# Kernel optimization log

Measured on AMD Instinct MI355X. Metric: run time of the kernel, lower is better.

The kernel has to match this reference:

```python
import jax, jax.numpy as jnp
import numpy as np

NEG_SLOPE = 0.2


def _gcn_conv(x, edge_index, W, b):
    # Standard GCNConv: y = D^-1/2 (A + I) D^-1/2 (x W) + b
    N = x.shape[0]
    loop = jnp.arange(N, dtype=edge_index.dtype)
    src = jnp.concatenate([edge_index[0], loop])  # [E+N]
    dst = jnp.concatenate([edge_index[1], loop])  # [E+N]
    deg = jax.ops.segment_sum(jnp.ones_like(dst, dtype=x.dtype), dst, num_segments=N)
    dinv = jnp.where(deg > 0, jax.lax.rsqrt(deg), 0.0)
    norm = dinv[src] * dinv[dst]                  # [E+N]
    h = x @ W                                     # [N, out] dense GEMM
    msg = h[src] * norm[:, None]                  # irregular gather, [E+N, out]
    agg = jax.ops.segment_sum(msg, dst, num_segments=N)  # irregular scatter
    return agg + b


def setup_inputs() -> dict:
    key = jax.random.key(0)
    ks = jax.random.split(key, 5)
    N, E, d_in, d_hid = 50000, 800000, 256, 512
    s = lambda fan_in, fan_out: np.sqrt(6.0 / (fan_in + fan_out))
    return {
        "x": jax.random.normal(ks[0], (N, d_in), dtype=jnp.float32),
        "edge_index": jax.random.randint(ks[1], (2, E), 0, N, dtype=jnp.int64),
        "W_gcn": jax.random.uniform(ks[2], (d_in, d_hid), jnp.float32, -s(d_in, d_hid), s(d_in, d_hid)),
        "b_gcn": jnp.zeros((d_hid,), jnp.float32),
        "W2": jax.random.uniform(ks[3], (d_hid, d_hid), jnp.float32, -s(d_hid, d_hid), s(d_hid, d_hid)),
        "b2": jnp.zeros((d_hid,), jnp.float32),
        "W_out": jax.random.uniform(ks[4], (d_hid, 1), jnp.float32, -s(d_hid, 1), s(d_hid, 1)),
        "b_out": jnp.zeros((1,), jnp.float32),
    }


def reference(x, edge_index, W_gcn, b_gcn, W2, b2, W_out, b_out):
    h = _gcn_conv(x, edge_index, W_gcn, b_gcn)           # [N, 512]
    h = jax.nn.leaky_relu(h, NEG_SLOPE)
    h = jax.nn.leaky_relu(h @ W2 + b2, NEG_SLOPE)        # [N, 512]
    return h @ W_out + b_out                             # [N, 1]
```

## Files before the change

kernel.cpp:

```cpp
#include <hip/hip_runtime.h>

#define D_IN  256
#define D_HID 512
#define NEG_SLOPE 0.2f
#define SCAN_CHUNK 2048

typedef __attribute__((ext_vector_type(8))) short short8;
typedef __attribute__((ext_vector_type(4))) float floatx4;

__device__ __forceinline__ unsigned short f2bf(float f) {
    unsigned int u = __float_as_uint(f);
    u += 0x7fffu + ((u >> 16) & 1u);
    return (unsigned short)(u >> 16);
}
__device__ __forceinline__ float bf2f(unsigned short u) {
    return __uint_as_float(((unsigned int)u) << 16);
}

__device__ __forceinline__ int eidx(const void* ei, long pos, int is64) {
    return is64 ? (int)((const long long*)ei)[pos] : ((const int*)ei)[pos];
}

__global__ __launch_bounds__(256) void k_init(const float* __restrict__ x,
                                              unsigned short* __restrict__ xb,
                                              int* __restrict__ deg, int N,
                                              const unsigned int* __restrict__ ei,
                                              int npairs, int* flag,
                                              const float* __restrict__ W_gcn,
                                              unsigned short* __restrict__ Wgt,
                                              const float* __restrict__ W2,
                                              unsigned short* __restrict__ W2t,
                                              const float* __restrict__ b_out,
                                              float* __restrict__ outacc,
                                              long xthreads) {
    long t = (long)blockIdx.x * blockDim.x + threadIdx.x;
    if (t < xthreads) {
        long i = t * 4;
        float4 v = *(const float4*)(x + i);
        ushort4 o;
        o.x = f2bf(v.x); o.y = f2bf(v.y); o.z = f2bf(v.z); o.w = f2bf(v.w);
        *(ushort4*)(xb + i) = o;
        if (t < N) deg[t] = 0;
        if (blockIdx.x == 0) {
            __shared__ int nz;
            if (threadIdx.x == 0) nz = 0;
            __syncthreads();
            for (int p = threadIdx.x; p < npairs; p += blockDim.x)
                if (ei[2 * p + 1] != 0) nz = 1;
            __syncthreads();
            if (threadIdx.x == 0) *flag = nz ? 0 : 1;
        }
        return;
    }
    long u = t - xthreads;
    if (u < (long)D_IN * D_HID) {
        int tt = (int)u;
        int n = tt / D_IN, k = tt - n * D_IN;
        Wgt[tt] = f2bf(W_gcn[(long)k * D_HID + n]);
        return;
    }
    u -= (long)D_IN * D_HID;
    if (u < (long)D_HID * D_HID) {
        int tt = (int)u;
        int n = tt / D_HID, k = tt - n * D_HID;
        W2t[tt] = f2bf(W2[(long)k * D_HID + n]);
        return;
    }
    u -= (long)D_HID * D_HID;
    if (u < N) outacc[u] = b_out[0];
}

__global__ void k_deg_count(const void* __restrict__ ei, const int* __restrict__ flag,
                            int* __restrict__ deg, int E) {
    int e = blockIdx.x * blockDim.x + threadIdx.x;
    if (e < E) atomicAdd(&deg[eidx(ei, (long)E + e, *flag)], 1);
}

__global__ __launch_bounds__(256) void k_scan1(const int* __restrict__ deg,
                                               int* __restrict__ bsum, int N) {
    int base = blockIdx.x * SCAN_CHUNK;
    int hi = min(base + SCAN_CHUNK, N);
    int s = 0;
    for (int i = base + threadIdx.x; i < hi; i += 256) s += deg[i];
#pragma unroll
    for (int off = 32; off > 0; off >>= 1) s += __shfl_down(s, off, 64);
    __shared__ int lds[4];
    if ((threadIdx.x & 63) == 0) lds[threadIdx.x >> 6] = s;
    __syncthreads();
    if (threadIdx.x == 0) bsum[blockIdx.x] = lds[0] + lds[1] + lds[2] + lds[3];
}

__global__ __launch_bounds__(256) void k_scan23(const int* __restrict__ deg,
                                                const int* __restrict__ bsum, int NB,
                                                int* __restrict__ offs,
                                                int* __restrict__ cursor,
                                                float* __restrict__ dinv, int N) {
    __shared__ int lds[256];
    int t = threadIdx.x;
    int bbase = 0;
    for (int i = 0; i < NB; ++i) bbase += (i < blockIdx.x) ? bsum[i] : 0;
    if (blockIdx.x == NB - 1 && t == 0) offs[N] = bbase + bsum[NB - 1];
    int base = blockIdx.x * SCAN_CHUNK;
    int lo = base + t * 8;
    int v[8], s = 0;
#pragma unroll
    for (int j = 0; j < 8; ++j) {
        int i = lo + j;
        v[j] = (i < N) ? deg[i] : 0;
        s += v[j];
    }
    lds[t] = s;
    __syncthreads();
    for (int d = 1; d < 256; d <<= 1) {
        int add = (t >= d) ? lds[t - d] : 0;
        __syncthreads();
        lds[t] += add;
        __syncthreads();
    }
    int run = bbase + ((t > 0) ? lds[t - 1] : 0);
#pragma unroll
    for (int j = 0; j < 8; ++j) {
        int i = lo + j;
        if (i < N) {
            offs[i] = run; cursor[i] = run;
            dinv[i] = rsqrtf(1.0f + (float)v[j]);
            run += v[j];
        }
    }
}

__global__ void k_fill(const void* __restrict__ ei, const int* __restrict__ flag,
                       int* __restrict__ cursor, int* __restrict__ esrc, int E) {
    int e = blockIdx.x * blockDim.x + threadIdx.x;
    if (e >= E) return;
    int is64 = *flag;
    int s = eidx(ei, e, is64), d = eidx(ei, (long)E + e, is64);
    int pos = atomicAdd(&cursor[d], 1);
    esrc[pos] = s;
}

__global__ __launch_bounds__(256) void k_gather(const unsigned short* __restrict__ xb,
                                                const int* __restrict__ offs,
                                                const int* __restrict__ esrc,
                                                const float* __restrict__ dinv,
                                                unsigned short* __restrict__ aggb, int N) {
    int node = blockIdx.x * 4 + (threadIdx.x >> 6);
    int lane = threadIdx.x & 63;
    if (node >= N) return;
    int half = lane >> 5;
    int li   = lane & 31;
    int colofs = li * 8;
    float di = dinv[node];

    float a[8];
    {
        short8 v = *(const short8*)(xb + (long)node * D_IN + colofs);
#pragma unroll
        for (int j = 0; j < 8; ++j)
            a[j] = (half == 0) ? di * bf2f((unsigned short)v[j]) : 0.f;
    }

    int beg = offs[node], end = offs[node + 1];
    int e = beg;
    for (; e + 8 <= end; e += 8) {
        int s0 = esrc[e + half];
        int s1 = esrc[e + 2 + half];
        int s2 = esrc[e + 4 + half];
        int s3 = esrc[e + 6 + half];
        float w0 = dinv[s0], w1 = dinv[s1], w2 = dinv[s2], w3 = dinv[s3];
        short8 u0 = *(const short8*)(xb + (long)s0 * D_IN + colofs);
        short8 u1 = *(const short8*)(xb + (long)s1 * D_IN + colofs);
        short8 u2 = *(const short8*)(xb + (long)s2 * D_IN + colofs);
        short8 u3 = *(const short8*)(xb + (long)s3 * D_IN + colofs);
#pragma unroll
        for (int j = 0; j < 8; ++j)
            a[j] += w0 * bf2f((unsigned short)u0[j]) + w1 * bf2f((unsigned short)u1[j])
                  + w2 * bf2f((unsigned short)u2[j]) + w3 * bf2f((unsigned short)u3[j]);
    }
    for (; e < end; e += 2) {
        int j0 = e + half;
        int jj = (j0 < end) ? j0 : end - 1;
        int s = esrc[jj];
        float w = (j0 < end) ? dinv[s] : 0.f;
        short8 u = *(const short8*)(xb + (long)s * D_IN + colofs);
#pragma unroll
        for (int j = 0; j < 8; ++j)
            a[j] += w * bf2f((unsigned short)u[j]);
    }

#pragma unroll
    for (int j = 0; j < 8; ++j) a[j] += __shfl_xor(a[j], 32, 64);

    if (half == 0) {
        short8 o;
#pragma unroll
        for (int j = 0; j < 8; ++j) o[j] = (short)f2bf(a[j] * di);
        *(short8*)(aggb + (long)node * D_IN + colofs) = o;
    }
}

__device__ __forceinline__ void async_cp16(const unsigned short* gp, unsigned short* lp) {
    __builtin_amdgcn_global_load_lds((const __attribute__((address_space(1))) void*)gp,
                                     (__attribute__((address_space(3))) void*)lp, 16, 0, 0);
}

__device__ __forceinline__ void stage_sw(const unsigned short* src, int strideK,
                                         int rowMax, unsigned short* lds, int tid) {
#pragma unroll
    for (int rr = 0; rr < 2; ++rr) {
        int c = rr * 256 + tid;
        int p = c >> 3;
        int ci = (c & 7) ^ (p & 7);
        int row = 2 * p + (ci >> 2);
        if (row > rowMax) row = rowMax;
        async_cp16(src + (long)row * strideK + (ci & 3) * 8, lds + c * 8);
    }
}

__device__ __forceinline__ bool map_block(int b, int M, int& m0, int& n0) {
    int x = b & 7, slot = b >> 3;
    int mt = x + 8 * (slot >> 2);
    m0 = mt * 128; n0 = (slot & 3) * 128;
    return m0 < M;
}

__global__ __launch_bounds__(256) void k_gemm_bf16(const unsigned short* __restrict__ A,
                                                   const unsigned short* __restrict__ Bt,
                                                   const float* __restrict__ bias,
                                                   unsigned short* __restrict__ C,
                                                   int M, int K) {
    __shared__ __align__(16) unsigned short As[128 * 32];
    __shared__ __align__(16) unsigned short Bs[128 * 32];
    __shared__ __align__(16) unsigned short Ep[32 * 128];
    const int tid  = threadIdx.x;
    const int lane = tid & 63, wave = tid >> 6;
    int m0, n0;
    if (!map_block(blockIdx.x, M, m0, n0)) return;
    const int r = lane & 15, q = lane >> 4;
    const int rh = r >> 1;
    const int sa = (((r & 1) << 2) | q) ^ rh;
    const int wm = (wave & 1) * 64, wn = (wave >> 1) * 64;
    const int band = wm >> 6;

    floatx4 acc[4][4];
#pragma unroll
    for (int i = 0; i < 4; ++i)
#pragma unroll
        for (int j = 0; j < 4; ++j) acc[i][j] = (floatx4){0.f, 0.f, 0.f, 0.f};

    for (int k0 = 0; k0 < K; k0 += 32) {
        stage_sw(A + (long)m0 * K + k0, K, M - 1 - m0, As, tid);
        stage_sw(Bt + (long)n0 * K + k0, K, 127, Bs, tid);
        __syncthreads();

        short8 af[4], bf[4];
#pragma unroll
        for (int i = 0; i < 4; ++i)
            af[i] = *(const short8*)(As + (wm / 2 + i * 8 + rh) * 64 + sa * 8);
#pragma unroll
        for (int j = 0; j < 4; ++j)
            bf[j] = *(const short8*)(Bs + (wn / 2 + j * 8 + rh) * 64 + sa * 8);
#pragma unroll
        for (int i = 0; i < 4; ++i)
#pragma unroll
            for (int j = 0; j < 4; ++j)
                acc[i][j] = __builtin_amdgcn_mfma_f32_16x16x32_bf16(af[i], bf[j], acc[i][j], 0, 0, 0);
        __syncthreads();
    }

    float bv[4];
#pragma unroll
    for (int j = 0; j < 4; ++j) bv[j] = bias[n0 + wn + j * 16 + r];

#pragma unroll
    for (int i = 0; i < 4; ++i) {
#pragma unroll
        for (int j = 0; j < 4; ++j) {
#pragma unroll
            for (int t2 = 0; t2 < 4; ++t2) {
                float v = acc[i][j][t2] + bv[j];
                v = v > 0.f ? v : NEG_SLOPE * v;
                Ep[(band * 16 + q * 4 + t2) * 128 + wn + j * 16 + r] = f2bf(v);
            }
        }
        __syncthreads();
#pragma unroll
        for (int rr = 0; rr < 2; ++rr) {
            int c = rr * 256 + tid;
            int lrow = c >> 4, ccol = c & 15;
            int grow = m0 + (lrow >> 4) * 64 + i * 16 + (lrow & 15);
            if (grow < M) {
                short8 v = *(const short8*)(Ep + lrow * 128 + ccol * 8);
                *(short8*)(C + (long)grow * D_HID + n0 + ccol * 8) = v;
            }
        }
        __syncthreads();
    }
}

__global__ __launch_bounds__(256) void k_gemm2f(const unsigned short* __restrict__ A,
                                                const unsigned short* __restrict__ Bt,
                                                const float* __restrict__ bias,
                                                const float* __restrict__ wout,
                                                float* __restrict__ outacc,
                                                int M, int K) {
    __shared__ __align__(16) unsigned short As[128 * 32];
    __shared__ __align__(16) unsigned short Bs[128 * 32];
    const int tid  = threadIdx.x;
    const int lane = tid & 63, wave = tid >> 6;
    int m0, n0;
    if (!map_block(blockIdx.x, M, m0, n0)) return;
    const int r = lane & 15, q = lane >> 4;
    const int rh = r >> 1;
    const int sa = (((r & 1) << 2) | q) ^ rh;
    const int wm = (wave & 1) * 64, wn = (wave >> 1) * 64;

    floatx4 acc[4][4];
#pragma unroll
    for (int i = 0; i < 4; ++i)
#pragma unroll
        for (int j = 0; j < 4; ++j) acc[i][j] = (floatx4){0.f, 0.f, 0.f, 0.f};

    for (int k0 = 0; k0 < K; k0 += 32) {
        stage_sw(A + (long)m0 * K + k0, K, M - 1 - m0, As, tid);
        stage_sw(Bt + (long)n0 * K + k0, K, 127, Bs, tid);
        __syncthreads();

        short8 af[4], bf[4];
#pragma unroll
        for (int i = 0; i < 4; ++i)
            af[i] = *(const short8*)(As + (wm / 2 + i * 8 + rh) * 64 + sa * 8);
#pragma unroll
        for (int j = 0; j < 4; ++j)
            bf[j] = *(const short8*)(Bs + (wn / 2 + j * 8 + rh) * 64 + sa * 8);
#pragma unroll
        for (int i = 0; i < 4; ++i)
#pragma unroll
            for (int j = 0; j < 4; ++j)
                acc[i][j] = __builtin_amdgcn_mfma_f32_16x16x32_bf16(af[i], bf[j], acc[i][j], 0, 0, 0);
        __syncthreads();
    }

    float bv[4], wv[4];
#pragma unroll
    for (int j = 0; j < 4; ++j) {
        int col = n0 + wn + j * 16 + r;
        bv[j] = bias[col];
        wv[j] = wout[col];
    }
#pragma unroll
    for (int i = 0; i < 4; ++i) {
#pragma unroll
        for (int t2 = 0; t2 < 4; ++t2) {
            float p = 0.f;
#pragma unroll
            for (int j = 0; j < 4; ++j) {
                float v = acc[i][j][t2] + bv[j];
                v = v > 0.f ? v : NEG_SLOPE * v;
                p += v * wv[j];
            }
            p += __shfl_xor(p, 8, 64);
            p += __shfl_xor(p, 4, 64);
            p += __shfl_xor(p, 2, 64);
            p += __shfl_xor(p, 1, 64);
            if (r == 0) {
                int row = m0 + wm + i * 16 + q * 4 + t2;
                if (row < M) atomicAdd(&outacc[row], p);
            }
        }
    }
}

__global__ void k_out(const float* __restrict__ outacc, float* __restrict__ out, int N) {
    int i = blockIdx.x * blockDim.x + threadIdx.x;
    if (i < N) out[i] = outacc[i];
}

extern "C" void kernel_launch(void* const* d_in, const int* in_sizes, int n_in,
                              void* d_out, int out_size, void* d_ws, size_t ws_size,
                              hipStream_t stream) {
    const float* x     = (const float*)d_in[0];
    const void*  ei    = d_in[1];
    const float* W_gcn = (const float*)d_in[2];
    const float* b_gcn = (const float*)d_in[3];
    const float* W2    = (const float*)d_in[4];
    const float* b2    = (const float*)d_in[5];
    const float* W_out = (const float*)d_in[6];
    const float* b_out = (const float*)d_in[7];
    float* out = (float*)d_out;

    const int N = in_sizes[0] / D_IN;
    const int E = in_sizes[1] / 2;
    const int NB = (N + SCAN_CHUNK - 1) / SCAN_CHUNK;

    char* w = (char*)d_ws;
    size_t off = 0;
    auto alloc = [&](size_t bytes) { char* p = w + off; off = (off + bytes + 255) & ~(size_t)255; return p; };
    int*            flag   = (int*)alloc(256);
    float*          dinv   = (float*)alloc((size_t)N * 4);
    int*            deg_i  = (int*)alloc((size_t)N * 4);
    int*            offs   = (int*)alloc((size_t)(N + 1) * 4);
    int*            cursor = (int*)alloc((size_t)N * 4);
    float*          outacc = (float*)alloc((size_t)N * 4);
    int*            bsum   = (int*)alloc((size_t)NB * 4);
    int*            esrc   = (int*)alloc((size_t)(E + 16) * 4);
    unsigned short* xb     = (unsigned short*)alloc((size_t)N * D_IN * 2);
    unsigned short* aggb   = (unsigned short*)alloc((size_t)N * D_IN * 2);
    unsigned short* h1     = (unsigned short*)alloc((size_t)N * D_HID * 2);
    unsigned short* Wgt    = (unsigned short*)alloc((size_t)D_IN * D_HID * 2);
    unsigned short* W2t    = (unsigned short*)alloc((size_t)D_HID * D_HID * 2);

    int npairs = E < 2048 ? E : 2048;
    long xthreads = ((long)N * D_IN) / 4;
    long prep_elems = (long)D_IN * D_HID + (long)D_HID * D_HID + N;
    long tot_threads = xthreads + prep_elems;
    k_init<<<(unsigned)((tot_threads + 255) / 256), 256, 0, stream>>>(
        x, xb, deg_i, N, (const unsigned int*)ei, npairs, flag,
        W_gcn, Wgt, W2, W2t, b_out, outacc, xthreads);

    k_deg_count<<<(E + 255) / 256, 256, 0, stream>>>(ei, flag, deg_i, E);
    k_scan1<<<NB, 256, 0, stream>>>(deg_i, bsum, N);
    k_scan23<<<NB, 256, 0, stream>>>(deg_i, bsum, NB, offs, cursor, dinv, N);
    k_fill<<<(E + 255) / 256, 256, 0, stream>>>(ei, flag, cursor, esrc, E);

    k_gather<<<(N + 3) / 4, 256, 0, stream>>>(xb, offs, esrc, dinv, aggb, N);

    int mtiles = (N + 127) / 128;
    int gblocks = ((mtiles + 7) / 8) * 8 * 4;
    k_gemm_bf16<<<gblocks, 256, 0, stream>>>(aggb, Wgt, b_gcn, h1, N, D_IN);
    k_gemm2f<<<gblocks, 256, 0, stream>>>(h1, W2t, b2, W_out, outacc, N, D_HID);

    k_out<<<(N + 255) / 256, 256, 0, stream>>>(outacc, out, N);
}
```

Measured before the change: 337.1 us.

## Fuse CSR build into one cooperative kernel with grid-wide syncs

Replaces the degree count, two scan kernels and the edge fill with a single cooperative kernel over a fixed 512-block grid that uses grid.sync between phases. The int64 detection moves from k_init into a per-wave ballot, and the block-offset prefix is done once by a single thread. The goal is to remove several launch gaps and the redundant per-block summation of block sums. The cost is grid-sync barriers, and grid-stride loops over 512 blocks may give less parallelism than the earlier one-thread-per-edge launches.

```diff
diff --git a/kernel.cpp b/kernel.cpp
--- a/kernel.cpp
+++ b/kernel.cpp
@@ -1,9 +1,13 @@
 #include <hip/hip_runtime.h>
+#include <hip/hip_cooperative_groups.h>
+
+namespace cg = cooperative_groups;
 
 #define D_IN  256
 #define D_HID 512
 #define NEG_SLOPE 0.2f
 #define SCAN_CHUNK 2048
+#define COOP_GRID 512
 
 typedef __attribute__((ext_vector_type(8))) short short8;
 typedef __attribute__((ext_vector_type(4))) float floatx4;
@@ -23,16 +27,13 @@
 
 __global__ __launch_bounds__(256) void k_init(const float* __restrict__ x,
                                               unsigned short* __restrict__ xb,
-                                              int* __restrict__ deg, int N,
-                                              const unsigned int* __restrict__ ei,
-                                              int npairs, int* flag,
                                               const float* __restrict__ W_gcn,
                                               unsigned short* __restrict__ Wgt,
                                               const float* __restrict__ W2,
                                               unsigned short* __restrict__ W2t,
                                               const float* __restrict__ b_out,
                                               float* __restrict__ outacc,
-                                              long xthreads) {
+                                              int N, long xthreads) {
     long t = (long)blockIdx.x * blockDim.x + threadIdx.x;
     if (t < xthreads) {
         long i = t * 4;
@@ -40,16 +41,6 @@
         ushort4 o;
         o.x = f2bf(v.x); o.y = f2bf(v.y); o.z = f2bf(v.z); o.w = f2bf(v.w);
         *(ushort4*)(xb + i) = o;
-        if (t < N) deg[t] = 0;
-        if (blockIdx.x == 0) {
-            __shared__ int nz;
-            if (threadIdx.x == 0) nz = 0;
-            __syncthreads();
-            for (int p = threadIdx.x; p < npairs; p += blockDim.x)
-                if (ei[2 * p + 1] != 0) nz = 1;
-            __syncthreads();
-            if (threadIdx.x == 0) *flag = nz ? 0 : 1;
-        }
         return;
     }
     long u = t - xthreads;
@@ -70,73 +61,94 @@
     if (u < N) outacc[u] = b_out[0];
 }
 
-__global__ void k_deg_count(const void* __restrict__ ei, const int* __restrict__ flag,
-                            int* __restrict__ deg, int E) {
-    int e = blockIdx.x * blockDim.x + threadIdx.x;
-    if (e < E) atomicAdd(&deg[eidx(ei, (long)E + e, *flag)], 1);
-}
-
-__global__ __launch_bounds__(256) void k_scan1(const int* __restrict__ deg,
-                                               int* __restrict__ bsum, int N) {
-    int base = blockIdx.x * SCAN_CHUNK;
-    int hi = min(base + SCAN_CHUNK, N);
-    int s = 0;
-    for (int i = base + threadIdx.x; i < hi; i += 256) s += deg[i];
-#pragma unroll
-    for (int off = 32; off > 0; off >>= 1) s += __shfl_down(s, off, 64);
-    __shared__ int lds[4];
-    if ((threadIdx.x & 63) == 0) lds[threadIdx.x >> 6] = s;
-    __syncthreads();
-    if (threadIdx.x == 0) bsum[blockIdx.x] = lds[0] + lds[1] + lds[2] + lds[3];
-}
-
-__global__ __launch_bounds__(256) void k_scan23(const int* __restrict__ deg,
-                                                const int* __restrict__ bsum, int NB,
-                                                int* __restrict__ offs,
-                                                int* __restrict__ cursor,
-                                                float* __restrict__ dinv, int N) {
-    __shared__ int lds[256];
-    int t = threadIdx.x;
-    int bbase = 0;
-    for (int i = 0; i < NB; ++i) bbase += (i < blockIdx.x) ? bsum[i] : 0;
-    if (blockIdx.x == NB - 1 && t == 0) offs[N] = bbase + bsum[NB - 1];
-    int base = blockIdx.x * SCAN_CHUNK;
-    int lo = base + t * 8;
-    int v[8], s = 0;
-#pragma unroll
-    for (int j = 0; j < 8; ++j) {
-        int i = lo + j;
-        v[j] = (i < N) ? deg[i] : 0;
-        s += v[j];
-    }
-    lds[t] = s;
-    __syncthreads();
-    for (int d = 1; d < 256; d <<= 1) {
-        int add = (t >= d) ? lds[t - d] : 0;
-        __syncthreads();
-        lds[t] += add;
-        __syncthreads();
-    }
-    int run = bbase + ((t > 0) ? lds[t - 1] : 0);
-#pragma unroll
-    for (int j = 0; j < 8; ++j) {
-        int i = lo + j;
-        if (i < N) {
-            offs[i] = run; cursor[i] = run;
-            dinv[i] = rsqrtf(1.0f + (float)v[j]);
-            run += v[j];
-        }
-    }
-}
-
-__global__ void k_fill(const void* __restrict__ ei, const int* __restrict__ flag,
-                       int* __restrict__ cursor, int* __restrict__ esrc, int E) {
-    int e = blockIdx.x * blockDim.x + threadIdx.x;
-    if (e >= E) return;
-    int is64 = *flag;
-    int s = eidx(ei, e, is64), d = eidx(ei, (long)E + e, is64);
-    int pos = atomicAdd(&cursor[d], 1);
-    esrc[pos] = s;
+__global__ __launch_bounds__(256, 2) void k_graph(const void* __restrict__ ei,
+                                                  int E, int N,
+                                                  int* __restrict__ deg,
+                                                  int* __restrict__ bsum,
+                                                  int* __restrict__ bbase,
+                                                  int* __restrict__ offs,
+                                                  int* __restrict__ cursor,
+                                                  float* __restrict__ dinv,
+                                                  int* __restrict__ esrc) {
+    cg::grid_group grid = cg::this_grid();
+    const int tid = threadIdx.x, bid = blockIdx.x;
+    const long gtid = (long)bid * 256 + tid;
+    const long gsz  = (long)gridDim.x * 256;
+    const int NBc = (N + SCAN_CHUNK - 1) / SCAN_CHUNK;
+
+    int is64;
+    {
+        const unsigned int* w = (const unsigned int*)ei;
+        unsigned int v = w[2 * (tid & 63) + 1];
+        unsigned long long m = __ballot(v != 0);
+        is64 = (m == 0ull) ? 1 : 0;
+    }
+
+    for (long i = gtid; i < N; i += gsz) deg[i] = 0;
+    grid.sync();
+
+    for (long e = gtid; e < E; e += gsz)
+        atomicAdd(&deg[eidx(ei, (long)E + e, is64)], 1);
+    grid.sync();
+
+    if (bid < NBc) {
+        int base = bid * SCAN_CHUNK;
+        int hi = min(base + SCAN_CHUNK, N);
+        int s = 0;
+        for (int i = base + tid; i < hi; i += 256) s += deg[i];
+#pragma unroll
+        for (int o = 32; o > 0; o >>= 1) s += __shfl_down(s, o, 64);
+        __shared__ int l4[4];
+        if ((tid & 63) == 0) l4[tid >> 6] = s;
+        __syncthreads();
+        if (tid == 0) bsum[bid] = l4[0] + l4[1] + l4[2] + l4[3];
+    }
+    grid.sync();
+
+    if (bid == 0 && tid == 0) {
+        int run = 0;
+        for (int i = 0; i < NBc; ++i) { bbase[i] = run; run += bsum[i]; }
+        offs[N] = run;
+    }
+    grid.sync();
+
+    if (bid < NBc) {
+        __shared__ int lds[256];
+        int base = bid * SCAN_CHUNK;
+        int lo = base + tid * 8;
+        int v[8], s = 0;
+#pragma unroll
+        for (int j = 0; j < 8; ++j) {
+            int i = lo + j;
+            v[j] = (i < N) ? deg[i] : 0;
+            s += v[j];
+        }
+        lds[tid] = s;
+        __syncthreads();
+        for (int d = 1; d < 256; d <<= 1) {
+            int add = (tid >= d) ? lds[tid - d] : 0;
+            __syncthreads();
+            lds[tid] += add;
+            __syncthreads();
+        }
+        int run = bbase[bid] + ((tid > 0) ? lds[tid - 1] : 0);
+#pragma unroll
+        for (int j = 0; j < 8; ++j) {
+            int i = lo + j;
+            if (i < N) {
+                offs[i] = run; cursor[i] = run;
+                dinv[i] = rsqrtf(1.0f + (float)v[j]);
+                run += v[j];
+            }
+        }
+    }
+    grid.sync();
+
+    for (long e = gtid; e < E; e += gsz) {
+        int s = eidx(ei, e, is64), d = eidx(ei, (long)E + e, is64);
+        int pos = atomicAdd(&cursor[d], 1);
+        esrc[pos] = s;
+    }
 }
 
 __global__ __launch_bounds__(256) void k_gather(const unsigned short* __restrict__ xb,
@@ -389,20 +401,20 @@
     const float* b_out = (const float*)d_in[7];
     float* out = (float*)d_out;
 
-    const int N = in_sizes[0] / D_IN;
-    const int E = in_sizes[1] / 2;
+    int N = in_sizes[0] / D_IN;
+    int E = in_sizes[1] / 2;
     const int NB = (N + SCAN_CHUNK - 1) / SCAN_CHUNK;
 
     char* w = (char*)d_ws;
     size_t off = 0;
     auto alloc = [&](size_t bytes) { char* p = w + off; off = (off + bytes + 255) & ~(size_t)255; return p; };
-    int*            flag   = (int*)alloc(256);
     float*          dinv   = (float*)alloc((size_t)N * 4);
     int*            deg_i  = (int*)alloc((size_t)N * 4);
     int*            offs   = (int*)alloc((size_t)(N + 1) * 4);
     int*            cursor = (int*)alloc((size_t)N * 4);
     float*          outacc = (float*)alloc((size_t)N * 4);
     int*            bsum   = (int*)alloc((size_t)NB * 4);
+    int*            bbase  = (int*)alloc((size_t)NB * 4);
     int*            esrc   = (int*)alloc((size_t)(E + 16) * 4);
     unsigned short* xb     = (unsigned short*)alloc((size_t)N * D_IN * 2);
     unsigned short* aggb   = (unsigned short*)alloc((size_t)N * D_IN * 2);
@@ -410,18 +422,16 @@
     unsigned short* Wgt    = (unsigned short*)alloc((size_t)D_IN * D_HID * 2);
     unsigned short* W2t    = (unsigned short*)alloc((size_t)D_HID * D_HID * 2);
 
-    int npairs = E < 2048 ? E : 2048;
     long xthreads = ((long)N * D_IN) / 4;
     long prep_elems = (long)D_IN * D_HID + (long)D_HID * D_HID + N;
     long tot_threads = xthreads + prep_elems;
     k_init<<<(unsigned)((tot_threads + 255) / 256), 256, 0, stream>>>(
-        x, xb, deg_i, N, (const unsigned int*)ei, npairs, flag,
-        W_gcn, Wgt, W2, W2t, b_out, outacc, xthreads);
-
-    k_deg_count<<<(E + 255) / 256, 256, 0, stream>>>(ei, flag, deg_i, E);
-    k_scan1<<<NB, 256, 0, stream>>>(deg_i, bsum, N);
-    k_scan23<<<NB, 256, 0, stream>>>(deg_i, bsum, NB, offs, cursor, dinv, N);
-    k_fill<<<(E + 255) / 256, 256, 0, stream>>>(ei, flag, cursor, esrc, E);
+        x, xb, W_gcn, Wgt, W2, W2t, b_out, outacc, N, xthreads);
+
+    void* kargs[] = { (void*)&ei, (void*)&E, (void*)&N, (void*)&deg_i, (void*)&bsum,
+                      (void*)&bbase, (void*)&offs, (void*)&cursor, (void*)&dinv, (void*)&esrc };
+    hipLaunchCooperativeKernel((const void*)k_graph, dim3(COOP_GRID), dim3(256),
+                               kargs, 0, stream);
 
     k_gather<<<(N + 3) / 4, 256, 0, stream>>>(xb, offs, esrc, dinv, aggb, N);
 
```

Result: slower. 618.5 us (+83.5%).
